# Kernel optimization log

Measured on AMD Instinct MI355X. Metric: run time of the kernel, lower is better.

Reference implementation:

```python
import jax, jax.numpy as jnp
import numpy as np

D = 768   # embedding_len
NL = 4    # nleft attributes
NR = 4    # nright attributes
LL = 256  # total left tokens
LR = 256  # total right tokens
DE = (NL + NR) * D  # entity-matching highway width


def setup_inputs() -> dict:
    key = jax.random.key(0)
    ks = jax.random.split(key, 12)
    f = lambda k, s: (jax.random.normal(k, s, jnp.float32) * 0.02)
    return {
        "left_emb": jax.random.normal(ks[0], (LL, D), jnp.float32),
        "right_emb": jax.random.normal(ks[1], (LR, D), jnp.float32),
        "Wn_tok": f(ks[2], (D, D)), "bn_tok": jnp.zeros((D,), jnp.float32),
        "Wg_tok": f(ks[3], (D, D)), "bg_tok": jnp.full((D,), -2.0, jnp.float32),
        "W_lin_tok": f(ks[4], (D, 1)), "b_lin_tok": jnp.zeros((1,), jnp.float32),
        "attr_emb_left": f(ks[5], (NL, D)),
        "attr_emb_right": f(ks[6], (NR, D)),
        "Wn_ent": f(ks[7], (DE, DE)), "bn_ent": jnp.zeros((DE,), jnp.float32),
        "Wg_ent": f(ks[8], (DE, DE)), "bg_ent": jnp.full((DE,), -2.0, jnp.float32),
        "W_lin_ent": f(ks[9], (DE, 2)), "b_lin_ent": jnp.zeros((2,), jnp.float32),
        "empty_attr_res": f(ks[10], (D,)),
        # per-attribute token counts; left includes an empty attribute
        "left_attrs_len": jnp.array([100, 80, 76, 0], dtype=jnp.int32),
        "right_attrs_len": jnp.array([64, 64, 64, 64], dtype=jnp.int32),
    }


def _highway(x, Wn, bn, Wg, bg):
    h = jax.nn.relu(x @ Wn + bn)
    g = jax.nn.sigmoid(x @ Wg + bg)
    return h * g + (1.0 - g) * x


def _token_matching(left, right, Wn, bn, Wg, bg, W_lin, b_lin):
    # compare_matrix: [L_left, L_right, D]
    cmp = jnp.abs(left[:, None, :] - right[None, :, :])
    hw = _highway(cmp, Wn, bn, Wg, bg)
    scores = hw @ W_lin + b_lin                     # [Ll, Lr, 1]
    # softmax over dim=1 (right tokens); only argmax is used downstream
    idx = jnp.argmax(scores[..., 0], axis=1)        # [Ll]
    return jnp.take_along_axis(cmp, idx[:, None, None], axis=1)[:, 0, :]  # [Ll, D]


def _attribute_matching(tokens, field_emb, cmp_res, lens, empty_attr):
    # ragged per-attribute softmax-weighted segment reduction
    n = field_emb.shape[0]
    L = tokens.shape[0]
    seg = jnp.repeat(jnp.arange(n), lens, total_repeat_length=L)   # [L]
    scores = jnp.einsum('ld,ld->l', tokens, field_emb[seg])        # [L]
    m = jax.ops.segment_max(scores, seg, num_segments=n)
    e = jnp.exp(scores - m[seg])
    z = jax.ops.segment_sum(e, seg, num_segments=n)
    w = e / z[seg]                                                  # softmax within segment
    reps = jax.ops.segment_sum(w[:, None] * cmp_res, seg, num_segments=n)  # [n, D]
    return jnp.where(lens[:, None] > 0, reps, empty_attr[None, :])


def reference(left_emb, right_emb, Wn_tok, bn_tok, Wg_tok, bg_tok,
              W_lin_tok, b_lin_tok, attr_emb_left, attr_emb_right,
              Wn_ent, bn_ent, Wg_ent, bg_ent, W_lin_ent, b_lin_ent,
              empty_attr_res, left_attrs_len, right_attrs_len):
    left_cmp = _token_matching(left_emb, right_emb, Wn_tok, bn_tok, Wg_tok, bg_tok,
                               W_lin_tok, b_lin_tok)
    right_cmp = _token_matching(right_emb, left_emb, Wn_tok, bn_tok, Wg_tok, bg_tok,
                                W_lin_tok, b_lin_tok)
    left_rep = _attribute_matching(left_emb, attr_emb_left, left_cmp,
                                   left_attrs_len, empty_attr_res)
    right_rep = _attribute_matching(right_emb, attr_emb_right, right_cmp,
                                    right_attrs_len, empty_attr_res)
    concat = jnp.concatenate([left_rep, right_rep], axis=0).reshape(1, -1)  # [1, DE]
    hw = _highway(concat, Wn_ent, bn_ent, Wg_ent, bg_ent)
    logits = hw @ W_lin_ent + b_lin_ent                                     # [1, 2]
    return jax.nn.softmax(logits, axis=1).flatten()                         # [2]
```

## Files before the change

kernel.cpp:

```cpp
#include <hip/hip_runtime.h>
#include <math.h>
#include <stdint.h>

#define DD 768
#define NT 256
#define DE 6144

typedef _Float16 half8 __attribute__((ext_vector_type(8)));
typedef float floatx4 __attribute__((ext_vector_type(4)));

__device__ __forceinline__ void async_ld16(const void* g, void* l) {
  __builtin_amdgcn_global_load_lds(
      (const __attribute__((address_space(1))) unsigned int*)g,
      (__attribute__((address_space(3))) unsigned int*)l, 16, 0, 0);
}

__global__ __launch_bounds__(256) void transpose_cvt(
    const float* __restrict__ Wn, const float* __restrict__ Wg,
    _Float16* __restrict__ WnT, _Float16* __restrict__ WgT)
{
  const float* W = blockIdx.z ? Wg : Wn;
  _Float16* WT = blockIdx.z ? WgT : WnT;
  __shared__ float tile[32][33];
  const int tx = threadIdx.x & 31, ty = threadIdx.x >> 5;
  const int d0 = blockIdx.x * 32, k0 = blockIdx.y * 32;
  #pragma unroll
  for (int p = 0; p < 4; ++p)
    tile[ty + p*8][tx] = W[(size_t)(k0 + ty + p*8)*DD + d0 + tx];
  __syncthreads();
  #pragma unroll
  for (int p = 0; p < 4; ++p) {
    const int d = d0 + ty + p*8;
    const int k = k0 + tx;
    const int idx = d*DD + (k & ~63) + ((((k >> 3) & 7) ^ (d & 7)) << 3) + (k & 7);
    WT[idx] = (_Float16)tile[tx][ty + p*8];
  }
}

__global__ __launch_bounds__(256, 2) void score_mfma(
    const float* __restrict__ L, const float* __restrict__ R,
    const _Float16* __restrict__ WnT, const _Float16* __restrict__ WgT,
    const float* __restrict__ bn, const float* __restrict__ bg,
    const float* __restrict__ Wl, float* __restrict__ S)
{
  const int jbase = blockIdx.x * 128;
  const int dbase = blockIdx.y * 128;
  const int i     = blockIdx.z;
  const int tid   = threadIdx.x;

  __shared__ _Float16 As [128*64];
  __shared__ _Float16 Bns[128*64];
  __shared__ _Float16 Bgs[128*64];

  floatx4 accn[4][4] = {};
  floatx4 accg[4][4] = {};

  const int kg = tid & 7;
  const int rl = tid >> 3;

  const int lane = tid & 63;
  const int wid  = tid >> 6;
  const int wj = (wid & 1) * 64;
  const int wd = (wid >> 1) * 64;
  const int m = lane & 15;
  const int q = lane >> 4;
  const int gq8 = ((q ^ (m & 7)) << 3);

  const int drow = lane >> 3;
  const int dseg = lane & 7;

  int aoff[4], boff[4];
  #pragma unroll
  for (int t4 = 0; t4 < 4; ++t4) {
    aoff[t4] = (wj + t4*16 + m) * 64;
    boff[t4] = (wd + t4*16 + m) * 64;
  }

  for (int k0 = 0; k0 < DD; k0 += 64) {
    #pragma unroll
    for (int t = 0; t < 4; ++t) {
      const int row = wid*32 + t*8 + drow;
      async_ld16(&WnT[(size_t)(dbase + row)*DD + k0 + dseg*8],
                 &Bns[(wid*32 + t*8)*64]);
      async_ld16(&WgT[(size_t)(dbase + row)*DD + k0 + dseg*8],
                 &Bgs[(wid*32 + t*8)*64]);
    }
    float l8[8];
    *(float4*)&l8[0] = *(const float4*)&L[i*DD + k0 + kg*8];
    *(float4*)&l8[4] = *(const float4*)&L[i*DD + k0 + kg*8 + 4];
    #pragma unroll
    for (int rep = 0; rep < 4; ++rep) {
      const int row = rl + rep*32;
      float rv[8];
      const float* Rrow = &R[(size_t)(jbase + row)*DD + k0 + kg*8];
      *(float4*)&rv[0] = *(const float4*)&Rrow[0];
      *(float4*)&rv[4] = *(const float4*)&Rrow[4];
      half8 h;
      #pragma unroll
      for (int e = 0; e < 8; ++e) h[e] = (_Float16)fabsf(l8[e] - rv[e]);
      *(half8*)&As[row*64 + ((kg ^ (row & 7)) << 3)] = h;
    }
    __syncthreads();
    #pragma unroll
    for (int kk = 0; kk < 64; kk += 32) {
      const int ko = kk ^ gq8;
      half8 af[4], bfn[4], bfg[4];
      #pragma unroll
      for (int t4 = 0; t4 < 4; ++t4) af[t4] = *(const half8*)&As[aoff[t4] + ko];
      #pragma unroll
      for (int t4 = 0; t4 < 4; ++t4) {
        bfn[t4] = *(const half8*)&Bns[boff[t4] + ko];
        bfg[t4] = *(const half8*)&Bgs[boff[t4] + ko];
      }
      #pragma unroll
      for (int tj = 0; tj < 4; ++tj)
        #pragma unroll
        for (int td = 0; td < 4; ++td) {
          accn[tj][td] = __builtin_amdgcn_mfma_f32_16x16x32_f16(
              af[tj], bfn[td], accn[tj][td], 0, 0, 0);
          accg[tj][td] = __builtin_amdgcn_mfma_f32_16x16x32_f16(
              af[tj], bfg[td], accg[tj][td], 0, 0, 0);
        }
    }
    __syncthreads();
  }

  float bnv[4], bgv[4], wlv[4], lv[4];
  int dv[4];
  #pragma unroll
  for (int td = 0; td < 4; ++td) {
    const int d = dbase + wd + td*16 + m;
    dv[td] = d; bnv[td] = bn[d]; bgv[td] = bg[d]; wlv[td] = Wl[d];
    lv[td] = L[i*DD + d];
  }
  const int jb = jbase + wj;
  #pragma unroll
  for (int tj = 0; tj < 4; ++tj) {
    #pragma unroll
    for (int r = 0; r < 4; ++r) {
      const int j = jb + tj*16 + q*4 + r;
      float sc = 0.f;
      #pragma unroll
      for (int td = 0; td < 4; ++td) {
        const float nv = accn[tj][td][r] + bnv[td];
        const float gp = accg[tj][td][r] + bgv[td];
        const float g  = 1.f / (1.f + __expf(-gp));
        const float c  = fabsf(lv[td] - R[(size_t)j*DD + dv[td]]);
        sc += (fmaxf(nv, 0.f)*g + (1.f - g)*c) * wlv[td];
      }
      sc += __shfl_xor(sc, 1, 16);
      sc += __shfl_xor(sc, 2, 16);
      sc += __shfl_xor(sc, 4, 16);
      sc += __shfl_xor(sc, 8, 16);
      if (m == 0) atomicAdd(&S[i*NT + j], sc);
    }
  }
}

__global__ __launch_bounds__(256) void argmax_kernel(const float* __restrict__ S,
    int* __restrict__ idxL, int* __restrict__ idxR)
{
  int b = blockIdx.x;
  int t = threadIdx.x;
  float v = (b < NT) ? S[b*NT + t] : S[t*NT + (b - NT)];
  int idx = t;
  #pragma unroll
  for (int mm = 1; mm < 64; mm <<= 1) {
    float ov = __shfl_xor(v, mm, 64);
    int   oi = __shfl_xor(idx, mm, 64);
    if (ov > v || (ov == v && oi < idx)) { v = ov; idx = oi; }
  }
  __shared__ float sv[4]; __shared__ int si[4];
  if ((t & 63) == 0) { sv[t>>6] = v; si[t>>6] = idx; }
  __syncthreads();
  if (t == 0) {
    #pragma unroll
    for (int w = 1; w < 4; ++w)
      if (sv[w] > v || (sv[w] == v && si[w] < idx)) { v = sv[w]; idx = si[w]; }
    if (b < NT) idxL[b] = idx; else idxR[b - NT] = idx;
  }
}

__global__ __launch_bounds__(256) void attr_score(
    const float* __restrict__ Lemb, const float* __restrict__ Remb,
    const float* __restrict__ AEl, const float* __restrict__ AEr,
    const int* __restrict__ lensL, const int* __restrict__ lensR,
    float* __restrict__ wS, int* __restrict__ segA)
{
  const int side = blockIdx.x;
  const float* tok = side ? Remb : Lemb;
  const float* AE  = side ? AEr  : AEl;
  const int* lens  = side ? lensR : lensL;
  const int t = threadIdx.x;
  const int c0 = lens[0], c1 = c0 + lens[1], c2 = c1 + lens[2];
  const int seg = (t < c0) ? 0 : (t < c1) ? 1 : (t < c2) ? 2 : 3;
  float s = 0.f;
  const float4* tr = (const float4*)&tok[(size_t)t*DD];
  const float4* ar = (const float4*)&AE[(size_t)seg*DD];
  for (int k = 0; k < DD/4; ++k) {
    float4 a = tr[k], b = ar[k];
    s += a.x*b.x + a.y*b.y + a.z*b.z + a.w*b.w;
  }
  __shared__ float scS[NT]; __shared__ int segS[NT];
  __shared__ float mS[4], zS[4];
  scS[t] = s; segS[t] = seg;
  __syncthreads();
  if (t < 4) {
    float m = -INFINITY;
    for (int u = 0; u < NT; ++u) if (segS[u] == t) m = fmaxf(m, scS[u]);
    mS[t] = m;
    float z = 0.f;
    for (int u = 0; u < NT; ++u) if (segS[u] == t) z += __expf(scS[u] - m);
    zS[t] = z;
  }
  __syncthreads();
  wS[side*NT + t] = __expf(s - mS[seg]) / zS[seg];
  segA[side*NT + t] = seg;
}

__global__ __launch_bounds__(256) void attr_reduce(
    const float* __restrict__ Lemb, const float* __restrict__ Remb,
    const int* __restrict__ lensL, const int* __restrict__ lensR,
    const int* __restrict__ idxL, const int* __restrict__ idxR,
    const float* __restrict__ wS, const int* __restrict__ segA,
    const float* __restrict__ empty, float* __restrict__ x)
{
  const int side = blockIdx.x;
  const float* tok = side ? Remb : Lemb;
  const float* oth = side ? Lemb : Remb;
  const int* lens  = side ? lensR : lensL;
  const int* idx   = side ? idxR  : idxL;
  const float* w   = wS + side*NT;
  const int* sg    = segA + side*NT;
  float* xo = x + side*4*DD;
  const int t = threadIdx.x;
  const int dl = t & 63, uq = t >> 6;
  const int d = blockIdx.y*64 + dl;
  float a0 = 0.f, a1 = 0.f, a2 = 0.f, a3 = 0.f;
  for (int u = uq*64; u < uq*64 + 64; ++u) {
    const float c = fabsf(tok[(size_t)u*DD + d] - oth[(size_t)idx[u]*DD + d]);
    const float wc = w[u] * c;
    const int s = sg[u];
    a0 += (s == 0) ? wc : 0.f;
    a1 += (s == 1) ? wc : 0.f;
    a2 += (s == 2) ? wc : 0.f;
    a3 += (s == 3) ? wc : 0.f;
  }
  __shared__ float red[4][4][64];
  red[uq][0][dl] = a0; red[uq][1][dl] = a1;
  red[uq][2][dl] = a2; red[uq][3][dl] = a3;
  __syncthreads();
  if (uq == 0) {
    #pragma unroll
    for (int s = 0; s < 4; ++s) {
      float v = red[0][s][dl] + red[1][s][dl] + red[2][s][dl] + red[3][s][dl];
      xo[s*DD + d] = (lens[s] > 0) ? v : empty[d];
    }
  }
}

__global__ __launch_bounds__(256) void ent_matvec4(
    const float* __restrict__ x,
    const float* __restrict__ Wn, const float* __restrict__ Wg,
    float* __restrict__ pn, float* __restrict__ pg)
{
  const float* W = blockIdx.z ? Wg : Wn;
  float* p = blockIdx.z ? pg : pn;
  __shared__ float xs[96];
  const int db = blockIdx.x;
  const int kb = blockIdx.y;
  const int tid = threadIdx.x;
  if (tid < 96) xs[tid] = x[kb*96 + tid];
  __syncthreads();
  const int col = db*1024 + tid*4;
  float4 a = {0.f,0.f,0.f,0.f};
  const size_t base = (size_t)kb*96*DE + col;
  #pragma unroll 8
  for (int kk = 0; kk < 96; ++kk) {
    const float xv = xs[kk];
    float4 w = *(const float4*)&W[base + (size_t)kk*DE];
    a.x = fmaf(xv, w.x, a.x); a.y = fmaf(xv, w.y, a.y);
    a.z = fmaf(xv, w.z, a.z); a.w = fmaf(xv, w.w, a.w);
  }
  *(float4*)&p[(size_t)kb*DE + col] = a;
}

__global__ __launch_bounds__(256) void ent_reduce(
    const float* __restrict__ pn, const float* __restrict__ pg,
    float* __restrict__ yn, float* __restrict__ yg)
{
  const int o = blockIdx.x*256 + threadIdx.x;
  float sn = 0.f, sg = 0.f;
  for (int kb = 0; kb < 64; ++kb) {
    sn += pn[(size_t)kb*DE + o];
    sg += pg[(size_t)kb*DE + o];
  }
  yn[o] = sn; yg[o] = sg;
}

__global__ __launch_bounds__(256) void final_kernel(
    const float* __restrict__ x, const float* __restrict__ yn,
    const float* __restrict__ yg, const float* __restrict__ bn,
    const float* __restrict__ bg, const float* __restrict__ Wl,
    const float* __restrict__ bl, float* __restrict__ out)
{
  const int tid = threadIdx.x;
  float a0 = 0.f, a1 = 0.f;
  for (int p = 0; p < DE/256; ++p) {
    int d = p*256 + tid;
    float n  = yn[d] + bn[d];
    float gp = yg[d] + bg[d];
    float h  = fmaxf(n, 0.f);
    float g  = 1.f / (1.f + __expf(-gp));
    float hw = h*g + (1.f - g)*x[d];
    a0 += hw * Wl[d*2 + 0];
    a1 += hw * Wl[d*2 + 1];
  }
  #pragma unroll
  for (int mm = 1; mm < 64; mm <<= 1) {
    a0 += __shfl_xor(a0, mm, 64);
    a1 += __shfl_xor(a1, mm, 64);
  }
  __shared__ float s0[4], s1[4];
  if ((tid & 63) == 0) { s0[tid>>6] = a0; s1[tid>>6] = a1; }
  __syncthreads();
  if (tid == 0) {
    for (int w = 1; w < 4; ++w) { a0 += s0[w]; a1 += s1[w]; }
    float l0 = a0 + bl[0], l1 = a1 + bl[1];
    float m = fmaxf(l0, l1);
    float e0 = __expf(l0 - m), e1 = __expf(l1 - m);
    out[0] = e0 / (e0 + e1);
    out[1] = e1 / (e0 + e1);
  }
}

extern "C" void kernel_launch(void* const* d_in, const int* in_sizes, int n_in,
                              void* d_out, int out_size, void* d_ws, size_t ws_size,
                              hipStream_t stream) {
  const float* Lemb   = (const float*)d_in[0];
  const float* Remb   = (const float*)d_in[1];
  const float* Wn_tok = (const float*)d_in[2];
  const float* bn_tok = (const float*)d_in[3];
  const float* Wg_tok = (const float*)d_in[4];
  const float* bg_tok = (const float*)d_in[5];
  const float* Wl_tok = (const float*)d_in[6];
  const float* AEl    = (const float*)d_in[8];
  const float* AEr    = (const float*)d_in[9];
  const float* Wn_ent = (const float*)d_in[10];
  const float* bn_ent = (const float*)d_in[11];
  const float* Wg_ent = (const float*)d_in[12];
  const float* bg_ent = (const float*)d_in[13];
  const float* Wl_ent = (const float*)d_in[14];
  const float* bl_ent = (const float*)d_in[15];
  const float* empty  = (const float*)d_in[16];
  const int*   lensL  = (const int*)d_in[17];
  const int*   lensR  = (const int*)d_in[18];

  char* ws = (char*)d_ws;
  float* S    = (float*)(ws + 0);
  int*  idxL  = (int*)  (ws + 262144);
  int*  idxR  = (int*)  (ws + 263168);
  float* x    = (float*)(ws + 264192);
  float* yn   = (float*)(ws + 288768);
  float* yg   = (float*)(ws + 313344);
  float* wSm  = (float*)(ws + 337920);
  int*  segA  = (int*)  (ws + 339968);
  _Float16* WnT = (_Float16*)(ws + 342016);
  _Float16* WgT = (_Float16*)(ws + 1521664);
  float* pn   = (float*)(ws + 2701312);
  float* pg   = (float*)(ws + 4274176);

  hipMemsetAsync(S, 0, (size_t)NT*NT*sizeof(float), stream);

  transpose_cvt<<<dim3(24, 24, 2), 256, 0, stream>>>(Wn_tok, Wg_tok, WnT, WgT);
  score_mfma<<<dim3(2, 6, NT), 256, 0, stream>>>(
      Lemb, Remb, WnT, WgT, bn_tok, bg_tok, Wl_tok, S);
  argmax_kernel<<<512, 256, 0, stream>>>(S, idxL, idxR);
  attr_score<<<2, 256, 0, stream>>>(Lemb, Remb, AEl, AEr, lensL, lensR, wSm, segA);
  attr_reduce<<<dim3(2, 12), 256, 0, stream>>>(
      Lemb, Remb, lensL, lensR, idxL, idxR, wSm, segA, empty, x);
  ent_matvec4<<<dim3(6, 64, 2), 256, 0, stream>>>(x, Wn_ent, Wg_ent, pn, pg);
  ent_reduce<<<24, 256, 0, stream>>>(pn, pg, yn, yg);
  final_kernel<<<1, 256, 0, stream>>>(
      x, yn, yg, bn_ent, bg_ent, Wl_ent, bl_ent, (float*)d_out);
}
```

Measured before the change: 667.1 us.

## Pre-convert embeddings to fp16, replace score atomics with partial planes, fuse argmax/attr

Adds a kernel that converts the left/right embeddings to fp16 once, so the score kernel loads half-width data and computes the absolute difference with an fp16 subtract and sign-bit mask instead of per-element fp32 conversion. The atomicAdd accumulation into S is replaced by plain stores into 12 per-(d-block, wave-pair) partial planes, which the argmax kernel sums. This removes the memset. The argmax and attribute-score kernels are merged into one launch, and the workspace is re-laid out so the partial planes alias pn/pg. The trade-off is lower precision in the residual term, since the fp32 embedding values are now rounded to fp16 before subtraction, plus extra reads of the partial planes during argmax.

```diff
diff --git a/kernel.cpp b/kernel.cpp
--- a/kernel.cpp
+++ b/kernel.cpp
@@ -7,6 +7,8 @@
 #define DE 6144
 
 typedef _Float16 half8 __attribute__((ext_vector_type(8)));
+typedef _Float16 half4 __attribute__((ext_vector_type(4)));
+typedef short short8 __attribute__((ext_vector_type(8)));
 typedef float floatx4 __attribute__((ext_vector_type(4)));
 
 __device__ __forceinline__ void async_ld16(const void* g, void* l) {
@@ -37,11 +39,24 @@
   }
 }
 
+__global__ __launch_bounds__(256) void cvt_lr(
+    const float* __restrict__ L, const float* __restrict__ R,
+    _Float16* __restrict__ Lh, _Float16* __restrict__ Rh)
+{
+  const float* src = blockIdx.y ? R : L;
+  _Float16* dst = blockIdx.y ? Rh : Lh;
+  const int o = blockIdx.x*1024 + threadIdx.x*4;
+  float4 v = *(const float4*)&src[o];
+  half4 h; h[0] = (_Float16)v.x; h[1] = (_Float16)v.y;
+  h[2] = (_Float16)v.z; h[3] = (_Float16)v.w;
+  *(half4*)&dst[o] = h;
+}
+
 __global__ __launch_bounds__(256, 2) void score_mfma(
-    const float* __restrict__ L, const float* __restrict__ R,
+    const _Float16* __restrict__ Lh, const _Float16* __restrict__ Rh,
     const _Float16* __restrict__ WnT, const _Float16* __restrict__ WgT,
     const float* __restrict__ bn, const float* __restrict__ bg,
-    const float* __restrict__ Wl, float* __restrict__ S)
+    const float* __restrict__ Wl, float* __restrict__ Sp)
 {
   const int jbase = blockIdx.x * 128;
   const int dbase = blockIdx.y * 128;
@@ -85,20 +100,15 @@
       async_ld16(&WgT[(size_t)(dbase + row)*DD + k0 + dseg*8],
                  &Bgs[(wid*32 + t*8)*64]);
     }
-    float l8[8];
-    *(float4*)&l8[0] = *(const float4*)&L[i*DD + k0 + kg*8];
-    *(float4*)&l8[4] = *(const float4*)&L[i*DD + k0 + kg*8 + 4];
+    half8 l8 = *(const half8*)&Lh[i*DD + k0 + kg*8];
     #pragma unroll
     for (int rep = 0; rep < 4; ++rep) {
       const int row = rl + rep*32;
-      float rv[8];
-      const float* Rrow = &R[(size_t)(jbase + row)*DD + k0 + kg*8];
-      *(float4*)&rv[0] = *(const float4*)&Rrow[0];
-      *(float4*)&rv[4] = *(const float4*)&Rrow[4];
-      half8 h;
-      #pragma unroll
-      for (int e = 0; e < 8; ++e) h[e] = (_Float16)fabsf(l8[e] - rv[e]);
-      *(half8*)&As[row*64 + ((kg ^ (row & 7)) << 3)] = h;
+      half8 rv = *(const half8*)&Rh[(size_t)(jbase + row)*DD + k0 + kg*8];
+      half8 dv8 = l8 - rv;
+      short8 sb; __builtin_memcpy(&sb, &dv8, 16);
+      sb &= (short)0x7FFF;
+      *(short8*)&As[row*64 + ((kg ^ (row & 7)) << 3)] = sb;
     }
     __syncthreads();
     #pragma unroll
@@ -131,9 +141,11 @@
   for (int td = 0; td < 4; ++td) {
     const int d = dbase + wd + td*16 + m;
     dv[td] = d; bnv[td] = bn[d]; bgv[td] = bg[d]; wlv[td] = Wl[d];
-    lv[td] = L[i*DD + d];
+    lv[td] = (float)Lh[i*DD + d];
   }
   const int jb = jbase + wj;
+  const int plane = blockIdx.y * 2 + (wid >> 1);
+  float* Sout = Sp + (size_t)plane * NT * NT + (size_t)i * NT;
   #pragma unroll
   for (int tj = 0; tj < 4; ++tj) {
     #pragma unroll
@@ -145,72 +157,76 @@
         const float nv = accn[tj][td][r] + bnv[td];
         const float gp = accg[tj][td][r] + bgv[td];
         const float g  = 1.f / (1.f + __expf(-gp));
-        const float c  = fabsf(lv[td] - R[(size_t)j*DD + dv[td]]);
+        const float c  = fabsf(lv[td] - (float)Rh[(size_t)j*DD + dv[td]]);
         sc += (fmaxf(nv, 0.f)*g + (1.f - g)*c) * wlv[td];
       }
       sc += __shfl_xor(sc, 1, 16);
       sc += __shfl_xor(sc, 2, 16);
       sc += __shfl_xor(sc, 4, 16);
       sc += __shfl_xor(sc, 8, 16);
-      if (m == 0) atomicAdd(&S[i*NT + j], sc);
-    }
-  }
-}
-
-__global__ __launch_bounds__(256) void argmax_kernel(const float* __restrict__ S,
-    int* __restrict__ idxL, int* __restrict__ idxR)
-{
-  int b = blockIdx.x;
-  int t = threadIdx.x;
-  float v = (b < NT) ? S[b*NT + t] : S[t*NT + (b - NT)];
-  int idx = t;
-  #pragma unroll
-  for (int mm = 1; mm < 64; mm <<= 1) {
-    float ov = __shfl_xor(v, mm, 64);
-    int   oi = __shfl_xor(idx, mm, 64);
-    if (ov > v || (ov == v && oi < idx)) { v = ov; idx = oi; }
-  }
-  __shared__ float sv[4]; __shared__ int si[4];
-  if ((t & 63) == 0) { sv[t>>6] = v; si[t>>6] = idx; }
-  __syncthreads();
-  if (t == 0) {
-    #pragma unroll
-    for (int w = 1; w < 4; ++w)
-      if (sv[w] > v || (sv[w] == v && si[w] < idx)) { v = sv[w]; idx = si[w]; }
-    if (b < NT) idxL[b] = idx; else idxR[b - NT] = idx;
-  }
-}
-
-__global__ __launch_bounds__(256) void attr_score(
+      if (m == 0) Sout[j] = sc;
+    }
+  }
+}
+
+__global__ __launch_bounds__(256) void argmax_attr(
+    const float* __restrict__ Sp,
+    int* __restrict__ idxL, int* __restrict__ idxR,
     const float* __restrict__ Lemb, const float* __restrict__ Remb,
     const float* __restrict__ AEl, const float* __restrict__ AEr,
     const int* __restrict__ lensL, const int* __restrict__ lensR,
     float* __restrict__ wS, int* __restrict__ segA)
 {
-  const int side = blockIdx.x;
+  const int b = blockIdx.x;
+  const int t = threadIdx.x;
+
+  if (b < 2*NT) {
+    const size_t off = (b < NT) ? ((size_t)b*NT + t) : ((size_t)t*NT + (b - NT));
+    float v = 0.f;
+    #pragma unroll
+    for (int p = 0; p < 12; ++p) v += Sp[(size_t)p*NT*NT + off];
+    int idx = t;
+    #pragma unroll
+    for (int mm = 1; mm < 64; mm <<= 1) {
+      float ov = __shfl_xor(v, mm, 64);
+      int   oi = __shfl_xor(idx, mm, 64);
+      if (ov > v || (ov == v && oi < idx)) { v = ov; idx = oi; }
+    }
+    __shared__ float sv[4]; __shared__ int si[4];
+    if ((t & 63) == 0) { sv[t>>6] = v; si[t>>6] = idx; }
+    __syncthreads();
+    if (t == 0) {
+      #pragma unroll
+      for (int w = 1; w < 4; ++w)
+        if (sv[w] > v || (sv[w] == v && si[w] < idx)) { v = sv[w]; idx = si[w]; }
+      if (b < NT) idxL[b] = idx; else idxR[b - NT] = idx;
+    }
+    return;
+  }
+
+  const int side = b - 2*NT;
   const float* tok = side ? Remb : Lemb;
   const float* AE  = side ? AEr  : AEl;
   const int* lens  = side ? lensR : lensL;
-  const int t = threadIdx.x;
   const int c0 = lens[0], c1 = c0 + lens[1], c2 = c1 + lens[2];
   const int seg = (t < c0) ? 0 : (t < c1) ? 1 : (t < c2) ? 2 : 3;
   float s = 0.f;
   const float4* tr = (const float4*)&tok[(size_t)t*DD];
   const float4* ar = (const float4*)&AE[(size_t)seg*DD];
   for (int k = 0; k < DD/4; ++k) {
-    float4 a = tr[k], b = ar[k];
-    s += a.x*b.x + a.y*b.y + a.z*b.z + a.w*b.w;
+    float4 a = tr[k], bb = ar[k];
+    s += a.x*bb.x + a.y*bb.y + a.z*bb.z + a.w*bb.w;
   }
   __shared__ float scS[NT]; __shared__ int segS[NT];
   __shared__ float mS[4], zS[4];
   scS[t] = s; segS[t] = seg;
   __syncthreads();
   if (t < 4) {
-    float m = -INFINITY;
-    for (int u = 0; u < NT; ++u) if (segS[u] == t) m = fmaxf(m, scS[u]);
-    mS[t] = m;
+    float mx = -INFINITY;
+    for (int u = 0; u < NT; ++u) if (segS[u] == t) mx = fmaxf(mx, scS[u]);
+    mS[t] = mx;
     float z = 0.f;
-    for (int u = 0; u < NT; ++u) if (segS[u] == t) z += __expf(scS[u] - m);
+    for (int u = 0; u < NT; ++u) if (segS[u] == t) z += __expf(scS[u] - mx);
     zS[t] = z;
   }
   __syncthreads();
@@ -357,26 +373,27 @@
   const int*   lensR  = (const int*)d_in[18];
 
   char* ws = (char*)d_ws;
-  float* S    = (float*)(ws + 0);
-  int*  idxL  = (int*)  (ws + 262144);
-  int*  idxR  = (int*)  (ws + 263168);
-  float* x    = (float*)(ws + 264192);
-  float* yn   = (float*)(ws + 288768);
-  float* yg   = (float*)(ws + 313344);
-  float* wSm  = (float*)(ws + 337920);
-  int*  segA  = (int*)  (ws + 339968);
-  _Float16* WnT = (_Float16*)(ws + 342016);
-  _Float16* WgT = (_Float16*)(ws + 1521664);
-  float* pn   = (float*)(ws + 2701312);
-  float* pg   = (float*)(ws + 4274176);
-
-  hipMemsetAsync(S, 0, (size_t)NT*NT*sizeof(float), stream);
+  float* Sp   = (float*)(ws + 0);
+  float* pn   = (float*)(ws + 0);
+  float* pg   = (float*)(ws + 1572864);
+  int*  idxL  = (int*)  (ws + 3145728);
+  int*  idxR  = (int*)  (ws + 3146752);
+  float* x    = (float*)(ws + 3147776);
+  float* yn   = (float*)(ws + 3172352);
+  float* yg   = (float*)(ws + 3196928);
+  float* wSm  = (float*)(ws + 3221504);
+  int*  segA  = (int*)  (ws + 3223552);
+  _Float16* WnT = (_Float16*)(ws + 3225600);
+  _Float16* WgT = (_Float16*)(ws + 4405248);
+  _Float16* Lh  = (_Float16*)(ws + 5584896);
+  _Float16* Rh  = (_Float16*)(ws + 5978112);
 
   transpose_cvt<<<dim3(24, 24, 2), 256, 0, stream>>>(Wn_tok, Wg_tok, WnT, WgT);
+  cvt_lr<<<dim3(192, 2), 256, 0, stream>>>(Lemb, Remb, Lh, Rh);
   score_mfma<<<dim3(2, 6, NT), 256, 0, stream>>>(
-      Lemb, Remb, WnT, WgT, bn_tok, bg_tok, Wl_tok, S);
-  argmax_kernel<<<512, 256, 0, stream>>>(S, idxL, idxR);
-  attr_score<<<2, 256, 0, stream>>>(Lemb, Remb, AEl, AEr, lensL, lensR, wSm, segA);
+      Lh, Rh, WnT, WgT, bn_tok, bg_tok, Wl_tok, Sp);
+  argmax_attr<<<514, 256, 0, stream>>>(
+      Sp, idxL, idxR, Lemb, Remb, AEl, AEr, lensL, lensR, wSm, segA);
   attr_reduce<<<dim3(2, 12), 256, 0, stream>>>(
       Lemb, Remb, lensL, lensR, idxL, idxR, wSm, segA, empty, x);
   ent_matvec4<<<dim3(6, 64, 2), 256, 0, stream>>>(x, Wn_ent, Wg_ent, pn, pg);
```

Measured after the change: 641.5 us. 3.8% less time.
